# Performance work log

Hardware: AMD Instinct MI355X
Metric: run time of the kernel (lower is better)

The kernel has to match this reference:

```python
import jax, jax.numpy as jnp
import numpy as np

S = 1024      # seq_len (capped by module's precomputed rows/cols tables)
B = 8         # batch
E = 512       # embed_dim
PD = 192      # pos_dim
H = 8         # num_heads
QHD = 32      # query_head_dim (== key_head_dim)
PHD = 4       # pos_head_dim
IN_DIM = (2 * QHD + PHD) * H  # 544


def setup_inputs() -> dict:
    key = jax.random.key(0)
    k0, k1, k2, k3 = jax.random.split(key, 4)
    x = jax.random.normal(k0, (S, B, E), jnp.float32)
    pos_emb = jax.random.normal(k1, (B, 2 * S - 1, PD), jnp.float32)
    # ScaledLinear(embed_dim, in_proj_dim, initial_scale=query_head_dim**-0.25)
    W_in = jax.random.normal(k2, (E, IN_DIM), jnp.float32) * (QHD ** -0.25) / np.sqrt(E).astype(np.float32)
    b_in = jnp.zeros((IN_DIM,), jnp.float32)
    # ScaledLinear(pos_dim, num_heads*pos_head_dim, bias=False, initial_scale=0.05)
    W_pos = jax.random.normal(k3, (PD, H * PHD), jnp.float32) * (0.05 / np.sqrt(PD).astype(np.float32))
    return {"x": x, "pos_emb": pos_emb, "W_in": W_in, "b_in": b_in, "W_pos": W_pos}


def reference(x, pos_emb, W_in, b_in, W_pos):
    s, b, _ = x.shape
    h, qhd, phd = H, QHD, PHD
    qdim = h * qhd

    proj = x @ W_in + b_in                      # [S, B, 544]
    q = proj[..., :qdim].reshape(s, b, h, qhd)          # [S,B,H,Dq]
    k = proj[..., qdim:2 * qdim].reshape(s, b, h, qhd)  # [S,B,H,Dq]
    p = proj[..., 2 * qdim:].reshape(s, b, h, phd)      # [S,B,H,Dp]

    # attn_scores[h,b,i,j] = q_i . k_j
    attn_scores = jnp.einsum('sbhd,tbhd->hbst', q, k)   # [H,B,S,S]

    # positional projection: [B, 2S-1, H, Dp]
    pe = (pos_emb @ W_pos).reshape(b, 2 * s - 1, h, phd)
    pos_scores = jnp.einsum('sbhd,bnhd->hbsn', p, pe)   # [H,B,S,2S-1]

    # relative skew: index[i,j] = (S-1-i) + j  (matches rows[-S:]+cols gather)
    idx = (s - 1) - jnp.arange(s)[:, None] + jnp.arange(s)[None, :]  # [S,S]
    idx_b = jnp.broadcast_to(idx[None, None], (h, b, s, s))
    rel = jnp.take_along_axis(pos_scores, idx_b, axis=-1)            # [H,B,S,S]

    return jax.nn.softmax(attn_scores + rel, axis=-1)
```

## Files before the change

kernel.cpp:

```cpp
#include <hip/hip_runtime.h>
#include <hip/hip_fp16.h>

#define S_LEN 1024
#define BATCH 8
#define EMB 512
#define POSD 192
#define NH 8
#define QHD 32
#define PHD 4
#define IN_DIM 544
#define QDIM 256
#define NPOS 2047

typedef _Float16 half8 __attribute__((ext_vector_type(8)));
typedef _Float16 half4_t __attribute__((ext_vector_type(4)));
typedef _Float16 half2_t __attribute__((ext_vector_type(2)));
typedef float f32x4 __attribute__((ext_vector_type(4)));

static __device__ __forceinline__ float fdot2(half2_t a, half2_t b, float c) {
#if __has_builtin(__builtin_amdgcn_fdot2)
  return __builtin_amdgcn_fdot2(a, b, c, false);
#else
  return c + (float)a[0] * (float)b[0] + (float)a[1] * (float)b[1];
#endif
}

__global__ __launch_bounds__(256) void prep_kernel(const float* __restrict__ W_in,
                                                   const float* __restrict__ W_pos,
                                                   const float* __restrict__ pos_emb,
                                                   _Float16* __restrict__ Wt,
                                                   _Float16* __restrict__ pe16) {
  __shared__ __align__(16) char smem[38400];
  const int blk = blockIdx.x;
  const int tid = threadIdx.x;
  if (blk < 72) {
    float (*T)[65] = reinterpret_cast<float(*)[65]>(smem);
    const int bx = blk % 9;
    const int by = blk / 9;
    const int n0 = bx * 64, e0 = by * 64;
    const int r = tid >> 4, c4 = (tid & 15) * 4;
    if (n0 + c4 < IN_DIM) {
      #pragma unroll
      for (int rr = 0; rr < 64; rr += 16) {
        f32x4 v = *(const f32x4*)(W_in + (size_t)(e0 + r + rr) * IN_DIM + n0 + c4);
        T[r + rr][c4] = v[0]; T[r + rr][c4 + 1] = v[1];
        T[r + rr][c4 + 2] = v[2]; T[r + rr][c4 + 3] = v[3];
      }
    }
    __syncthreads();
    const int nl = tid >> 2, ec = (tid & 3) * 16;
    const int n = n0 + nl;
    if (n < IN_DIM) {
      half8 h0, h1;
      #pragma unroll
      for (int j = 0; j < 8; ++j) {
        h0[j] = (_Float16)T[ec + j][nl];
        h1[j] = (_Float16)T[ec + 8 + j][nl];
      }
      *(half8*)(Wt + (size_t)n * EMB + e0 + ec) = h0;
      *(half8*)(Wt + (size_t)n * EMB + e0 + ec + 8) = h1;
    }
  } else {
    _Float16 (*As)[200] = reinterpret_cast<_Float16(*)[200]>(smem);
    _Float16 (*Wl)[200] = reinterpret_cast<_Float16(*)[200]>(smem + 25600);
    const int id = blk - 72;
    const int chunk = id & 31, b = id >> 5;
    const int n0 = chunk * 64;
    #pragma unroll
    for (int p = 0; p < 6; ++p) {
      int f = (p * 256 + tid) * 4;
      f32x4 v = *(const f32x4*)(W_pos + f);
      int k = f >> 5, c = f & 31;
      #pragma unroll
      for (int t = 0; t < 4; ++t) Wl[c + t][k] = (_Float16)v[t];
    }
    const int row = tid >> 2, sc = tid & 3;
    const bool rowok = (n0 + row) < NPOS;
    const float* src = pos_emb + ((size_t)b * NPOS + n0 + row) * POSD + sc * 48;
    #pragma unroll
    for (int j = 0; j < 6; ++j) {
      f32x4 v0 = {}, v1 = {};
      if (rowok) { v0 = *(const f32x4*)(src + j * 8); v1 = *(const f32x4*)(src + j * 8 + 4); }
      half8 h;
      #pragma unroll
      for (int t = 0; t < 4; ++t) { h[t] = (_Float16)v0[t]; h[4 + t] = (_Float16)v1[t]; }
      *(half8*)&As[row][sc * 48 + j * 8] = h;
    }
    __syncthreads();
    const int w = tid >> 6, l = tid & 63, g = l >> 4, lg = l & 15;
    f32x4 acc0 = {}, acc1 = {};
    #pragma unroll
    for (int kk = 0; kk < POSD; kk += 32) {
      half8 aF = *(const half8*)&As[w * 16 + lg][kk + g * 8];
      half8 b0 = *(const half8*)&Wl[lg][kk + g * 8];
      half8 b1 = *(const half8*)&Wl[16 + lg][kk + g * 8];
      acc0 = __builtin_amdgcn_mfma_f32_16x16x32_f16(aF, b0, acc0, 0, 0, 0);
      acc1 = __builtin_amdgcn_mfma_f32_16x16x32_f16(aF, b1, acc1, 0, 0, 0);
    }
    f32x4 accs[2] = {acc0, acc1};
    #pragma unroll
    for (int t = 0; t < 2; ++t) {
      int c = t * 16 + lg, h = c >> 2, d = c & 3;
      _Float16* dst = pe16 + ((size_t)(b * NH + h) * NPOS) * PHD + d;
      #pragma unroll
      for (int r2 = 0; r2 < 4; ++r2) {
        int n = n0 + w * 16 + 4 * g + r2;
        if (n < NPOS) dst[(size_t)n * PHD] = (_Float16)accs[t][r2];
      }
    }
  }
}

__global__ __launch_bounds__(256) void proj_kernel(const float* __restrict__ x,
                                                   const _Float16* __restrict__ Wt,
                                                   const float* __restrict__ bias,
                                                   _Float16* __restrict__ q16,
                                                   _Float16* __restrict__ k16,
                                                   _Float16* __restrict__ p16) {
  __shared__ __align__(16) _Float16 As[64][40];
  __shared__ __align__(16) _Float16 Bs[64][40];
  const int bid = blockIdx.x;
  const int xcd = bid & 7, idx = bid >> 3;
  const int mt = xcd * 16 + (idx & 15);
  const int nt = idx >> 4;
  const int m0 = mt * 64;
  const int n0 = nt * 64;
  const int tid = threadIdx.x;
  const int w = tid >> 6, l = tid & 63, g = l >> 4, lg = l & 15;
  const int wm = w >> 1, wn = w & 1;
  const int srow = tid >> 2, sc = tid & 3;

  f32x4 acc[2][2] = {};

  for (int k0 = 0; k0 < EMB; k0 += 32) {
    const float* asrc = x + (size_t)(m0 + srow) * EMB + k0 + sc * 8;
    f32x4 a0 = *(const f32x4*)asrc;
    f32x4 a1 = *(const f32x4*)(asrc + 4);
    half8 ah;
    #pragma unroll
    for (int j = 0; j < 4; ++j) { ah[j] = (_Float16)a0[j]; ah[4 + j] = (_Float16)a1[j]; }
    int nrow = n0 + srow;
    half8 bh8 = {};
    if (nrow < IN_DIM) bh8 = *(const half8*)(Wt + (size_t)nrow * EMB + k0 + sc * 8);
    *(half8*)&As[srow][sc * 8] = ah;
    *(half8*)&Bs[srow][sc * 8] = bh8;
    __syncthreads();
    half8 aF0 = *(const half8*)&As[wm * 32 + lg][g * 8];
    half8 aF1 = *(const half8*)&As[wm * 32 + 16 + lg][g * 8];
    half8 bF0 = *(const half8*)&Bs[wn * 32 + lg][g * 8];
    half8 bF1 = *(const half8*)&Bs[wn * 32 + 16 + lg][g * 8];
    acc[0][0] = __builtin_amdgcn_mfma_f32_16x16x32_f16(aF0, bF0, acc[0][0], 0, 0, 0);
    acc[0][1] = __builtin_amdgcn_mfma_f32_16x16x32_f16(aF0, bF1, acc[0][1], 0, 0, 0);
    acc[1][0] = __builtin_amdgcn_mfma_f32_16x16x32_f16(aF1, bF0, acc[1][0], 0, 0, 0);
    acc[1][1] = __builtin_amdgcn_mfma_f32_16x16x32_f16(aF1, bF1, acc[1][1], 0, 0, 0);
    __syncthreads();
  }

  #pragma unroll
  for (int sm = 0; sm < 2; ++sm)
    #pragma unroll
    for (int sn = 0; sn < 2; ++sn)
      #pragma unroll
      for (int r = 0; r < 4; ++r) {
        int m = m0 + wm * 32 + sm * 16 + 4 * g + r;
        int n = n0 + wn * 32 + sn * 16 + lg;
        if (n < IN_DIM) {
          float v = acc[sm][sn][r] + bias[n];
          _Float16 hv = (_Float16)v;
          int s = m >> 3, b = m & 7;
          if (n < QDIM) {
            int h = n >> 5, d = n & 31;
            q16[(((size_t)(b * NH + h)) * S_LEN + s) * QHD + d] = hv;
          } else if (n < 2 * QDIM) {
            int n2 = n - QDIM;
            int h = n2 >> 5, d = n2 & 31;
            k16[(((size_t)(b * NH + h)) * S_LEN + s) * QHD + d] = hv;
          } else {
            int n2 = n - 2 * QDIM;
            int h = n2 >> 2, d = n2 & 3;
            p16[(((size_t)(b * NH + h)) * S_LEN + s) * PHD + d] = hv;
          }
        }
      }
}

__global__ __launch_bounds__(256, 4) void attn_kernel(const _Float16* __restrict__ q16,
                                                      const _Float16* __restrict__ k16,
                                                      const _Float16* __restrict__ p16,
                                                      const _Float16* __restrict__ pe16,
                                                      float* __restrict__ out) {
  __shared__ __align__(16) _Float16 peLDS[1040 * 4];
  __shared__ float wred[4][16];
  __shared__ __align__(16) float sbuf[4][16][68];
  const int bid = blockIdx.x;
  const int swz = (bid & 7) * 512 + (bid >> 3);
  const int bh = swz >> 6;
  const int rblk = swz & 63;
  const int b = bh >> 3, h = bh & 7;
  const int i0 = rblk * 16;
  const int tid = threadIdx.x;
  const int w = tid >> 6, l = tid & 63, g = l >> 4, lg = l & 15;
  const int nlo = S_LEN - 16 - i0;

  for (int it = tid; it < 1039; it += 256) {
    *(uint2*)&peLDS[it * 4] =
        *(const uint2*)&pe16[((size_t)bh * NPOS + nlo + it) * 4];
  }

  const _Float16* qbase = q16 + ((size_t)bh * S_LEN + i0) * QHD;
  half8 qF = *(const half8*)(qbase + lg * QHD + g * 8);

  const _Float16* pbase = p16 + ((size_t)bh * S_LEN + i0 + lg) * PHD;
  half2_t pq0 = *(const half2_t*)(pbase);
  half2_t pq1 = *(const half2_t*)(pbase + 2);

  __syncthreads();

  const _Float16* kbase = k16 + (size_t)bh * S_LEN * QHD;
  const int jw = w * 256;
  f32x4 zero = {};
  float s = 0.f;
  half4_t probs[16];

  #pragma unroll
  for (int ct = 0; ct < 16; ++ct) {
    int j = jw + ct * 16 + lg;
    half8 kF = *(const half8*)(kbase + (size_t)j * QHD + g * 8);
    f32x4 a = __builtin_amdgcn_mfma_f32_16x16x32_f16(kF, qF, zero, 0, 0, 0);
    int nl0 = 15 - lg + jw + ct * 16 + 4 * g;
    half4_t ph;
    #pragma unroll
    for (int r = 0; r < 4; ++r) {
      half4_t pv4 = *(const half4_t*)&peLDS[(nl0 + r) * 4];
      half2_t lo = {pv4[0], pv4[1]};
      half2_t hi = {pv4[2], pv4[3]};
      float sc = fdot2(pq1, hi, fdot2(pq0, lo, a[r]));
      float e = __expf(sc - 6.0f);
      s += e;
      ph[r] = (_Float16)e;
    }
    probs[ct] = ph;
  }

  s += __shfl_xor(s, 16);
  s += __shfl_xor(s, 32);
  if (g == 0) wred[w][lg] = s;
  __syncthreads();
  s = (wred[0][lg] + wred[1][lg]) + (wred[2][lg] + wred[3][lg]);
  const float inv = 1.0f / s;

  const size_t orow0 = ((size_t)(h * BATCH + b) * S_LEN + i0) * S_LEN;
  #pragma unroll
  for (int chunk = 0; chunk < 4; ++chunk) {
    #pragma unroll
    for (int cc = 0; cc < 4; ++cc) {
      half4_t ph = probs[chunk * 4 + cc];
      f32x4 v;
      #pragma unroll
      for (int r = 0; r < 4; ++r) v[r] = (float)ph[r] * inv;
      *(f32x4*)&sbuf[w][lg][cc * 16 + 4 * g] = v;
    }
    asm volatile("s_waitcnt lgkmcnt(0)" ::: "memory");
    __builtin_amdgcn_sched_barrier(0);
    #pragma unroll
    for (int k2 = 0; k2 < 4; ++k2) {
      int rr = k2 * 4 + g;
      f32x4 v = *(const f32x4*)&sbuf[w][rr][lg * 4];
      __builtin_nontemporal_store(
          v, (f32x4*)(out + orow0 + (size_t)rr * S_LEN + jw + chunk * 64 + lg * 4));
    }
    asm volatile("s_waitcnt lgkmcnt(0)" ::: "memory");
    __builtin_amdgcn_sched_barrier(0);
  }
}

extern "C" void kernel_launch(void* const* d_in, const int* in_sizes, int n_in,
                              void* d_out, int out_size, void* d_ws, size_t ws_size,
                              hipStream_t stream) {
  const float* x = (const float*)d_in[0];
  const float* pos_emb = (const float*)d_in[1];
  const float* W_in = (const float*)d_in[2];
  const float* b_in = (const float*)d_in[3];
  const float* W_pos = (const float*)d_in[4];
  float* out = (float*)d_out;

  char* ws = (char*)d_ws;
  _Float16* Wt = (_Float16*)(ws);
  _Float16* q16 = (_Float16*)(ws + 557056);
  _Float16* k16 = (_Float16*)(ws + 557056 + 4194304);
  _Float16* p16 = (_Float16*)(ws + 557056 + 2 * 4194304);
  _Float16* pe16 = (_Float16*)(ws + 557056 + 2 * 4194304 + 524288);

  prep_kernel<<<dim3(328), dim3(256), 0, stream>>>(W_in, W_pos, pos_emb, Wt, pe16);
  proj_kernel<<<dim3(1152), dim3(256), 0, stream>>>(x, Wt, b_in, q16, k16, p16);
  attn_kernel<<<dim3(4096), dim3(256), 0, stream>>>(q16, k16, p16, pe16, out);
}
```

Baseline: 82.39 us.

## Fuse weight transpose and projection GEMM into one kernel with pos-emb prep

Removes the separate W_in transpose/fp16-conversion pass. The projection GEMM now reads fp32 W_in directly, converts it in registers, and gathers B fragments from LDS with strided scalar reads. The projection and pos-emb projection blocks are merged into one launch, which saves a kernel launch and the Wt round-trip through memory. In exchange, each projection block re-converts W_in and does per-element LDS reads for the B operand, which may cause bank conflicts.

```diff
diff --git a/kernel.cpp b/kernel.cpp
--- a/kernel.cpp
+++ b/kernel.cpp
@@ -25,45 +25,96 @@
 #endif
 }
 
-__global__ __launch_bounds__(256) void prep_kernel(const float* __restrict__ W_in,
-                                                   const float* __restrict__ W_pos,
-                                                   const float* __restrict__ pos_emb,
-                                                   _Float16* __restrict__ Wt,
-                                                   _Float16* __restrict__ pe16) {
+__global__ __launch_bounds__(256) void fused_kernel(const float* __restrict__ x,
+                                                    const float* __restrict__ W_in,
+                                                    const float* __restrict__ W_pos,
+                                                    const float* __restrict__ pos_emb,
+                                                    const float* __restrict__ bias,
+                                                    _Float16* __restrict__ q16,
+                                                    _Float16* __restrict__ k16,
+                                                    _Float16* __restrict__ p16,
+                                                    _Float16* __restrict__ pe16) {
   __shared__ __align__(16) char smem[38400];
-  const int blk = blockIdx.x;
+  const int bid = blockIdx.x;
   const int tid = threadIdx.x;
-  if (blk < 72) {
-    float (*T)[65] = reinterpret_cast<float(*)[65]>(smem);
-    const int bx = blk % 9;
-    const int by = blk / 9;
-    const int n0 = bx * 64, e0 = by * 64;
-    const int r = tid >> 4, c4 = (tid & 15) * 4;
-    if (n0 + c4 < IN_DIM) {
-      #pragma unroll
-      for (int rr = 0; rr < 64; rr += 16) {
-        f32x4 v = *(const f32x4*)(W_in + (size_t)(e0 + r + rr) * IN_DIM + n0 + c4);
-        T[r + rr][c4] = v[0]; T[r + rr][c4 + 1] = v[1];
-        T[r + rr][c4 + 2] = v[2]; T[r + rr][c4 + 3] = v[3];
+  if (bid < 1152) {
+    _Float16 (*As)[72] = reinterpret_cast<_Float16(*)[72]>(smem);
+    _Float16 (*Bs)[66] = reinterpret_cast<_Float16(*)[66]>(smem + 9216);
+    const int xcd = bid & 7, idx = bid >> 3;
+    const int mt = xcd * 16 + (idx & 15);
+    const int nt = idx >> 4;
+    const int m0 = mt * 64, n0 = nt * 64;
+    const int w = tid >> 6, l = tid & 63, g = l >> 4, lg = l & 15;
+    const int wm = w >> 1, wn = w & 1;
+    const int srow = tid >> 2, sc = tid & 3;
+    const int erow = tid >> 3, nc = (tid & 7) * 8;
+    const bool bok = (n0 + nc) < IN_DIM;
+
+    f32x4 acc[2][2] = {};
+
+    for (int k0 = 0; k0 < EMB; k0 += 32) {
+      const float* asrc = x + (size_t)(m0 + srow) * EMB + k0 + sc * 8;
+      f32x4 a0 = *(const f32x4*)asrc;
+      f32x4 a1 = *(const f32x4*)(asrc + 4);
+      half8 ah;
+      #pragma unroll
+      for (int j = 0; j < 4; ++j) { ah[j] = (_Float16)a0[j]; ah[4 + j] = (_Float16)a1[j]; }
+      half8 bh8 = {};
+      if (bok) {
+        const float* bsrc = W_in + (size_t)(k0 + erow) * IN_DIM + n0 + nc;
+        f32x4 b0 = *(const f32x4*)bsrc;
+        f32x4 b1 = *(const f32x4*)(bsrc + 4);
+        #pragma unroll
+        for (int j = 0; j < 4; ++j) { bh8[j] = (_Float16)b0[j]; bh8[4 + j] = (_Float16)b1[j]; }
       }
-    }
-    __syncthreads();
-    const int nl = tid >> 2, ec = (tid & 3) * 16;
-    const int n = n0 + nl;
-    if (n < IN_DIM) {
-      half8 h0, h1;
+      __syncthreads();
+      *(half8*)&As[srow][sc * 8] = ah;
+      *(half8*)&Bs[erow][nc] = bh8;
+      __syncthreads();
+      half8 aF0 = *(const half8*)&As[wm * 32 + lg][g * 8];
+      half8 aF1 = *(const half8*)&As[wm * 32 + 16 + lg][g * 8];
+      half8 bF0, bF1;
       #pragma unroll
       for (int j = 0; j < 8; ++j) {
-        h0[j] = (_Float16)T[ec + j][nl];
-        h1[j] = (_Float16)T[ec + 8 + j][nl];
+        bF0[j] = Bs[g * 8 + j][wn * 32 + lg];
+        bF1[j] = Bs[g * 8 + j][wn * 32 + 16 + lg];
       }
-      *(half8*)(Wt + (size_t)n * EMB + e0 + ec) = h0;
-      *(half8*)(Wt + (size_t)n * EMB + e0 + ec + 8) = h1;
-    }
+      acc[0][0] = __builtin_amdgcn_mfma_f32_16x16x32_f16(aF0, bF0, acc[0][0], 0, 0, 0);
+      acc[0][1] = __builtin_amdgcn_mfma_f32_16x16x32_f16(aF0, bF1, acc[0][1], 0, 0, 0);
+      acc[1][0] = __builtin_amdgcn_mfma_f32_16x16x32_f16(aF1, bF0, acc[1][0], 0, 0, 0);
+      acc[1][1] = __builtin_amdgcn_mfma_f32_16x16x32_f16(aF1, bF1, acc[1][1], 0, 0, 0);
+    }
+
+    #pragma unroll
+    for (int sm = 0; sm < 2; ++sm)
+      #pragma unroll
+      for (int sn = 0; sn < 2; ++sn)
+        #pragma unroll
+        for (int r = 0; r < 4; ++r) {
+          int m = m0 + wm * 32 + sm * 16 + 4 * g + r;
+          int n = n0 + wn * 32 + sn * 16 + lg;
+          if (n < IN_DIM) {
+            float v = acc[sm][sn][r] + bias[n];
+            _Float16 hv = (_Float16)v;
+            int s = m >> 3, b = m & 7;
+            if (n < QDIM) {
+              int h = n >> 5, d = n & 31;
+              q16[(((size_t)(b * NH + h)) * S_LEN + s) * QHD + d] = hv;
+            } else if (n < 2 * QDIM) {
+              int n2 = n - QDIM;
+              int h = n2 >> 5, d = n2 & 31;
+              k16[(((size_t)(b * NH + h)) * S_LEN + s) * QHD + d] = hv;
+            } else {
+              int n2 = n - 2 * QDIM;
+              int h = n2 >> 2, d = n2 & 3;
+              p16[(((size_t)(b * NH + h)) * S_LEN + s) * PHD + d] = hv;
+            }
+          }
+        }
   } else {
     _Float16 (*As)[200] = reinterpret_cast<_Float16(*)[200]>(smem);
     _Float16 (*Wl)[200] = reinterpret_cast<_Float16(*)[200]>(smem + 25600);
-    const int id = blk - 72;
+    const int id = bid - 1152;
     const int chunk = id & 31, b = id >> 5;
     const int n0 = chunk * 64;
     #pragma unroll
@@ -109,79 +160,6 @@
       }
     }
   }
-}
-
-__global__ __launch_bounds__(256) void proj_kernel(const float* __restrict__ x,
-                                                   const _Float16* __restrict__ Wt,
-                                                   const float* __restrict__ bias,
-                                                   _Float16* __restrict__ q16,
-                                                   _Float16* __restrict__ k16,
-                                                   _Float16* __restrict__ p16) {
-  __shared__ __align__(16) _Float16 As[64][40];
-  __shared__ __align__(16) _Float16 Bs[64][40];
-  const int bid = blockIdx.x;
-  const int xcd = bid & 7, idx = bid >> 3;
-  const int mt = xcd * 16 + (idx & 15);
-  const int nt = idx >> 4;
-  const int m0 = mt * 64;
-  const int n0 = nt * 64;
-  const int tid = threadIdx.x;
-  const int w = tid >> 6, l = tid & 63, g = l >> 4, lg = l & 15;
-  const int wm = w >> 1, wn = w & 1;
-  const int srow = tid >> 2, sc = tid & 3;
-
-  f32x4 acc[2][2] = {};
-
-  for (int k0 = 0; k0 < EMB; k0 += 32) {
-    const float* asrc = x + (size_t)(m0 + srow) * EMB + k0 + sc * 8;
-    f32x4 a0 = *(const f32x4*)asrc;
-    f32x4 a1 = *(const f32x4*)(asrc + 4);
-    half8 ah;
-    #pragma unroll
-    for (int j = 0; j < 4; ++j) { ah[j] = (_Float16)a0[j]; ah[4 + j] = (_Float16)a1[j]; }
-    int nrow = n0 + srow;
-    half8 bh8 = {};
-    if (nrow < IN_DIM) bh8 = *(const half8*)(Wt + (size_t)nrow * EMB + k0 + sc * 8);
-    *(half8*)&As[srow][sc * 8] = ah;
-    *(half8*)&Bs[srow][sc * 8] = bh8;
-    __syncthreads();
-    half8 aF0 = *(const half8*)&As[wm * 32 + lg][g * 8];
-    half8 aF1 = *(const half8*)&As[wm * 32 + 16 + lg][g * 8];
-    half8 bF0 = *(const half8*)&Bs[wn * 32 + lg][g * 8];
-    half8 bF1 = *(const half8*)&Bs[wn * 32 + 16 + lg][g * 8];
-    acc[0][0] = __builtin_amdgcn_mfma_f32_16x16x32_f16(aF0, bF0, acc[0][0], 0, 0, 0);
-    acc[0][1] = __builtin_amdgcn_mfma_f32_16x16x32_f16(aF0, bF1, acc[0][1], 0, 0, 0);
-    acc[1][0] = __builtin_amdgcn_mfma_f32_16x16x32_f16(aF1, bF0, acc[1][0], 0, 0, 0);
-    acc[1][1] = __builtin_amdgcn_mfma_f32_16x16x32_f16(aF1, bF1, acc[1][1], 0, 0, 0);
-    __syncthreads();
-  }
-
-  #pragma unroll
-  for (int sm = 0; sm < 2; ++sm)
-    #pragma unroll
-    for (int sn = 0; sn < 2; ++sn)
-      #pragma unroll
-      for (int r = 0; r < 4; ++r) {
-        int m = m0 + wm * 32 + sm * 16 + 4 * g + r;
-        int n = n0 + wn * 32 + sn * 16 + lg;
-        if (n < IN_DIM) {
-          float v = acc[sm][sn][r] + bias[n];
-          _Float16 hv = (_Float16)v;
-          int s = m >> 3, b = m & 7;
-          if (n < QDIM) {
-            int h = n >> 5, d = n & 31;
-            q16[(((size_t)(b * NH + h)) * S_LEN + s) * QHD + d] = hv;
-          } else if (n < 2 * QDIM) {
-            int n2 = n - QDIM;
-            int h = n2 >> 5, d = n2 & 31;
-            k16[(((size_t)(b * NH + h)) * S_LEN + s) * QHD + d] = hv;
-          } else {
-            int n2 = n - 2 * QDIM;
-            int h = n2 >> 2, d = n2 & 3;
-            p16[(((size_t)(b * NH + h)) * S_LEN + s) * PHD + d] = hv;
-          }
-        }
-      }
 }
 
 __global__ __launch_bounds__(256, 4) void attn_kernel(const _Float16* __restrict__ q16,
@@ -285,13 +263,12 @@
   float* out = (float*)d_out;
 
   char* ws = (char*)d_ws;
-  _Float16* Wt = (_Float16*)(ws);
   _Float16* q16 = (_Float16*)(ws + 557056);
   _Float16* k16 = (_Float16*)(ws + 557056 + 4194304);
   _Float16* p16 = (_Float16*)(ws + 557056 + 2 * 4194304);
   _Float16* pe16 = (_Float16*)(ws + 557056 + 2 * 4194304 + 524288);
 
-  prep_kernel<<<dim3(328), dim3(256), 0, stream>>>(W_in, W_pos, pos_emb, Wt, pe16);
-  proj_kernel<<<dim3(1152), dim3(256), 0, stream>>>(x, Wt, b_in, q16, k16, p16);
+  fused_kernel<<<dim3(1408), dim3(256), 0, stream>>>(x, W_in, W_pos, pos_emb, b_in,
+                                                     q16, k16, p16, pe16);
   attn_kernel<<<dim3(4096), dim3(256), 0, stream>>>(q16, k16, p16, pe16, out);
 }
```

After: 91.24 us. 1.11x slower.
